# Kernel optimization log

Measured on AMD Instinct MI355X. Metric: run time of the kernel, lower is better.

The kernel has to match this reference:

```python
import jax, jax.numpy as jnp
import numpy as np

HEADS = 4
DIM_HEAD = 64
KS = 7
IN_CH = 256
OUT_CH = HEADS * DIM_HEAD


def setup_inputs() -> dict:
    key = jax.random.key(0)
    k1, k2, k3, k4, k5 = jax.random.split(key, 5)
    b, c, h, w = 2, IN_CH, 64, 64
    kvmap1 = jax.random.normal(k1, (b, c, h, w), dtype=jnp.float32)
    qmap = jax.random.normal(k2, (b, c, h, w), dtype=jnp.float32)
    kvmap2 = jax.random.normal(k3, (b, c, h, w), dtype=jnp.float32)
    # 1x1 conv weights [out_channels, in_channels], kaiming-ish scale
    Wq = jax.random.normal(k4, (OUT_CH, IN_CH), dtype=jnp.float32) * (1.0 / np.sqrt(IN_CH))
    Wkv = jax.random.normal(k5, (OUT_CH, IN_CH), dtype=jnp.float32) * (1.0 / np.sqrt(IN_CH))
    return {"kvmap1": kvmap1, "qmap": qmap, "kvmap2": kvmap2, "Wq": Wq, "Wkv": Wkv}


def _branch(kvmap, Wkv, q, h, w):
    # pad like F.pad([ks//2, (ks-1)//2, ks//2, (ks-1)//2])
    pl, pr = KS // 2, (KS - 1) // 2
    padded = jnp.pad(kvmap, ((0, 0), (0, 0), (pl, pr), (pl, pr)))
    kv = jnp.einsum('bchw,oc->bohw', padded, Wkv)  # 1x1 conv, k == v in the original
    b = kv.shape[0]
    # unfold: [b, C, ks*ks, h, w] with (k1, k2) row-major, matching torch unfold order
    patches = jnp.stack([kv[:, :, i:i + h, j:j + w]
                         for i in range(KS) for j in range(KS)], axis=2)
    k = patches.reshape(b, HEADS, DIM_HEAD, KS * KS, h * w)
    k = k.transpose(0, 1, 4, 3, 2)  # [b, n, hw, k^2, d]
    logits = jnp.einsum('bnxd,bnxyd->bnxy', q, k)
    wts = jax.nn.softmax(logits, axis=-1)
    return jnp.einsum('bnxy,bnxyd->bnxd', wts, k)  # v == k


def reference(kvmap1, qmap, kvmap2, Wq, Wkv):
    b, c, h, w = qmap.shape
    scale = DIM_HEAD ** (-0.5)
    q = jnp.einsum('bchw,oc->bohw', qmap, Wq) * scale
    q = q.reshape(b, HEADS, DIM_HEAD, h * w).transpose(0, 1, 3, 2)  # [b, n, hw, d]
    out1 = _branch(kvmap1, Wkv, q, h, w)
    out2 = _branch(kvmap2, Wkv, q, h, w)
    out = (out1 + out2) * 0.5  # [b, n, hw, d]
    return out.transpose(0, 1, 3, 2).reshape(b, HEADS * DIM_HEAD, h, w)
```

## Files before the change

kernel.cpp:

```cpp
#include <hip/hip_runtime.h>
#include <hip/hip_bf16.h>
#include <math.h>

#define HEADS 4
#define DH 64
#define CH 256
#define HW 4096
#define HH 64
#define WW 64
#define BB 2
#define KS 7

#define NPOS 224
#define ROWB 448
#define WROWB 256

typedef __attribute__((ext_vector_type(8))) short bf16x8;
typedef __attribute__((ext_vector_type(4))) float f32x4;
typedef __attribute__((ext_vector_type(4))) short short4_t;

__device__ __forceinline__ short f2bf(float x) {
  union { float f; unsigned u; } v; v.f = x;
  unsigned r = (v.u + 0x7fffu + ((v.u >> 16) & 1u)) >> 16;
  return (short)r;
}

__device__ __forceinline__ int swz(int row, int byte_off) {
  return byte_off ^ ((row & 7) << 4);
}

__global__ __launch_bounds__(256) void wcvt_kernel(
    const float* __restrict__ Wq, const float* __restrict__ Wkv,
    short* __restrict__ Wqb, short* __restrict__ Wkvb) {
  const int i = (blockIdx.x * 256 + threadIdx.x) * 4;
  const float* src = blockIdx.y ? Wkv : Wq;
  short* dst = blockIdx.y ? Wkvb : Wqb;
  const float sc = blockIdx.y ? 1.0f : 0.125f;
  float4 v = *(const float4*)(src + i);
  short4_t o;
  o.x = f2bf(v.x * sc); o.y = f2bf(v.y * sc);
  o.z = f2bf(v.z * sc); o.w = f2bf(v.w * sc);
  *(short4_t*)(dst + i) = o;
}

__global__ __launch_bounds__(256) void proj_mfma_kernel(
    const float* __restrict__ qmap, const float* __restrict__ kvmap1,
    const float* __restrict__ kvmap2, const short* __restrict__ Wqb,
    const short* __restrict__ Wkvb, short* __restrict__ Qt,
    short* __restrict__ KV1, short* __restrict__ KV2) {
  const float* in; const short* Wb; short* out;
  switch (blockIdx.z >> 2) {
    case 0:  in = qmap;   Wb = Wqb;  out = Qt;  break;
    case 1:  in = kvmap1; Wb = Wkvb; out = KV1; break;
    default: in = kvmap2; Wb = Wkvb; out = KV2; break;
  }
  __shared__ short wl[64 * 256];
  const int ng = blockIdx.z & 3;
  const int b = blockIdx.y, t = threadIdx.x;
  const int w = t >> 6, lane = t & 63, l15 = lane & 15, lg = lane >> 4;

  {
    const short* wsrc = Wb + (size_t)(ng * 64) * CH;
    #pragma unroll
    for (int i = 0; i < 8; ++i) {
      int idx = i * 256 + t;
      int o = idx >> 5, slot = idx & 31;
      bf16x8 v = *(const bf16x8*)(wsrc + o * CH + slot * 8);
      *(bf16x8*)((char*)wl + o * 512 + ((slot * 16) ^ ((o & 7) * 16))) = v;
    }
  }

  const int pix = blockIdx.x * 64 + w * 16 + l15;
  const float* inb = in + (size_t)b * CH * HW;
  bf16x8 a[8];
  #pragma unroll
  for (int k8 = 0; k8 < 8; ++k8) {
    #pragma unroll
    for (int j = 0; j < 8; ++j)
      a[k8][j] = f2bf(inb[(size_t)(k8 * 32 + lg * 8 + j) * HW + pix]);
  }
  __syncthreads();

  const int prow = blockIdx.x * 64 + w * 16 + lg * 4;
  short* ob = out + (size_t)b * HW * CH;
  #pragma unroll
  for (int nq = 0; nq < 4; ++nq) {
    const int nt = ng * 4 + nq;
    const int o = nq * 16 + l15;
    f32x4 acc = (f32x4)0.f;
    #pragma unroll
    for (int k8 = 0; k8 < 8; ++k8) {
      bf16x8 bfrag = *(const bf16x8*)((char*)wl + o * 512 +
                                      (((k8 * 4 + lg) * 16) ^ ((o & 7) * 16)));
      acc = __builtin_amdgcn_mfma_f32_16x16x32_bf16(a[k8], bfrag, acc, 0, 0, 0);
    }
    #pragma unroll
    for (int r = 0; r < 4; ++r)
      ob[(size_t)(prow + r) * CH + nt * 16 + l15] = f2bf(acc[r]);
  }
}

__global__ __launch_bounds__(256, 3) void attn_kernel(
    const short* __restrict__ Qt, const short* __restrict__ KV1,
    const short* __restrict__ KV2, float* __restrict__ out) {
  __shared__ char KVT[64 * ROWB];
  __shared__ char WT [64 * WROWB];

  const int t = threadIdx.x, lane = t & 63, w = t >> 6;
  const int l15 = lane & 15, lg = lane >> 4;
  const int tile = blockIdx.x;
  const int ty = tile >> 3, tx = tile & 7;
  const int bn = blockIdx.y, b = bn >> 2, n = bn & 3;

  bf16x8 qf0, qf1;
  {
    int p = w * 16 + l15;
    int gp = (ty * 8 + (p >> 3)) * 64 + tx * 8 + (p & 7);
    const short* qb = Qt + ((size_t)b * HW + gp) * CH + n * DH + lg * 8;
    qf0 = *(const bf16x8*)(qb);
    qf1 = *(const bf16x8*)(qb + 32);
  }

  f32x4 acc2[4];
  #pragma unroll
  for (int i = 0; i < 4; ++i) acc2[i] = (f32x4)0.f;

  const int p = w * 16 + l15, px = p & 7;
  const int hi8 = l15 >> 3;

  #pragma unroll
  for (int br = 0; br < 2; ++br) {
    const short* kv = (br ? KV2 : KV1) + (size_t)b * HW * CH + n * DH;
    if (br) __syncthreads();

    #pragma unroll
    for (int it = 0; it < 2; ++it) {
      int tid = it * 256 + t;
      if (tid < 448) {
        int dc = (tid * 586) >> 15;
        int posT = tid - dc * 56;
        int pos0 = posT * 4;
        int uy = pos0 >> 4, ux0 = pos0 & 15;
        int gy = ty * 8 + uy - 3;
        bool yok = (gy >= 0) && (gy < HH);
        bf16x8 v[4];
        #pragma unroll
        for (int r = 0; r < 4; ++r) {
          int ux = ux0 + r;
          int gx = tx * 8 + ux - 3;
          bool valid = yok && (ux < 14) && (gx >= 0) && (gx < WW);
          v[r] = (bf16x8)0;
          if (valid)
            v[r] = *(const bf16x8*)(kv + (size_t)(gy * WW + gx) * CH + dc * 8);
        }
        #pragma unroll
        for (int j = 0; j < 8; ++j) {
          int d = dc * 8 + j;
          short4_t pk;
          pk[0] = v[0][j]; pk[1] = v[1][j]; pk[2] = v[2][j]; pk[3] = v[3][j];
          *(short4_t*)(KVT + swz(d, d * ROWB + pos0 * 2)) = pk;
        }
      }
    }
    __syncthreads();

    f32x4 sa[8];
    {
      int ux = l15;
      int gx = tx * 8 + ux - 3;
      bool xok = (ux < 14) && (gx >= 0) && (gx < WW);
      #pragma unroll
      for (int i = 0; i < 8; ++i) {
        int gy = ty * 8 + (2 * w + i) - 3;
        bool valid = xok && (gy >= 0) && (gy < HH);
        bf16x8 a0 = (bf16x8)0, a1 = (bf16x8)0;
        if (valid) {
          const short* src = kv + (size_t)(gy * WW + gx) * CH + lg * 8;
          a0 = *(const bf16x8*)(src);
          a1 = *(const bf16x8*)(src + 32);
        }
        f32x4 s = (f32x4)0.f;
        s = __builtin_amdgcn_mfma_f32_16x16x32_bf16(a0, qf0, s, 0, 0, 0);
        s = __builtin_amdgcn_mfma_f32_16x16x32_bf16(a1, qf1, s, 0, 0, 0);
        sa[i] = s;
      }
    }

    float m = -1e30f;
    #pragma unroll
    for (int i = 0; i < 8; ++i) {
      int dy = i - hi8;
      bool yok = (dy >= 0) && (dy <= 6);
      #pragma unroll
      for (int r = 0; r < 4; ++r) {
        int dx = (lg * 4 + r) - px;
        bool in = yok && (dx >= 0) && (dx <= 6);
        float s = in ? sa[i][r] : -1e30f;
        sa[i][r] = s;
        m = fmaxf(m, s);
      }
    }
    m = fmaxf(m, __shfl_xor(m, 16, 64));
    m = fmaxf(m, __shfl_xor(m, 32, 64));
    float den = 0.f;
    #pragma unroll
    for (int i = 0; i < 8; ++i) {
      #pragma unroll
      for (int r = 0; r < 4; ++r) {
        float e = __expf(sa[i][r] - m);
        sa[i][r] = e;
        den += e;
      }
    }
    den += __shfl_xor(den, 16, 64);
    den += __shfl_xor(den, 32, 64);
    float inv = 1.f / den;

    #pragma unroll
    for (int i = 0; i < 8; ++i) {
      short4_t pk;
      #pragma unroll
      for (int r = 0; r < 4; ++r) pk[r] = f2bf(sa[i][r] * inv);
      *(short4_t*)(WT + swz(p, p * WROWB + (i * 16 + lg * 4) * 2)) = pk;
    }

    #pragma unroll 1
    for (int kp = 0; kp < 4; ++kp) {
      int lposb = (kp * 32 + lg * 8) * 2;
      int gposb = (32 * w + kp * 32 + lg * 8) * 2;
      bf16x8 af = *(const bf16x8*)(WT + swz(p, p * WROWB + lposb));
      #pragma unroll
      for (int ntp = 0; ntp < 4; ++ntp) {
        int brow = ntp * 16 + l15;
        bf16x8 bf = *(const bf16x8*)(KVT + swz(brow, brow * ROWB + gposb));
        acc2[ntp] = __builtin_amdgcn_mfma_f32_16x16x32_bf16(af, bf, acc2[ntp], 0, 0, 0);
      }
    }
  }

  int p0 = w * 16 + lg * 4;
  int gp = (ty * 8 + (p0 >> 3)) * 64 + tx * 8 + (p0 & 7);
  #pragma unroll
  for (int ntp = 0; ntp < 4; ++ntp) {
    int o = n * DH + ntp * 16 + l15;
    f32x4 v = acc2[ntp] * 0.5f;
    *(f32x4*)(out + ((size_t)b * CH + o) * HW + gp) = v;
  }
}

extern "C" void kernel_launch(void* const* d_in, const int* in_sizes, int n_in,
                              void* d_out, int out_size, void* d_ws, size_t ws_size,
                              hipStream_t stream) {
  const float* kvmap1 = (const float*)d_in[0];
  const float* qmap   = (const float*)d_in[1];
  const float* kvmap2 = (const float*)d_in[2];
  const float* Wq     = (const float*)d_in[3];
  const float* Wkv    = (const float*)d_in[4];
  float* out = (float*)d_out;

  short* Qt   = (short*)d_ws;
  short* KV1  = Qt  + (size_t)BB * HW * CH;
  short* KV2  = KV1 + (size_t)BB * HW * CH;
  short* Wqb  = KV2 + (size_t)BB * HW * CH;
  short* Wkvb = Wqb + (size_t)CH * CH;

  dim3 wgrid(64, 2);
  wcvt_kernel<<<wgrid, 256, 0, stream>>>(Wq, Wkv, Wqb, Wkvb);

  dim3 pgrid(HW / 64, BB, 12);
  proj_mfma_kernel<<<pgrid, 256, 0, stream>>>(qmap, kvmap1, kvmap2, Wqb, Wkvb,
                                              Qt, KV1, KV2);

  dim3 agrid(64, BB * HEADS);
  attn_kernel<<<agrid, 256, 0, stream>>>(Qt, KV1, KV2, out);
}
```

Baseline: 40.12 us.

## Fuse weight conversion into projection and keep softmax weights in registers

```diff
diff --git a/kernel.cpp b/kernel.cpp
--- a/kernel.cpp
+++ b/kernel.cpp
@@ -1,5 +1,4 @@
 #include <hip/hip_runtime.h>
-#include <hip/hip_bf16.h>
 #include <math.h>
 
 #define HEADS 4
@@ -9,11 +8,9 @@
 #define HH 64
 #define WW 64
 #define BB 2
-#define KS 7
 
 #define NPOS 224
 #define ROWB 448
-#define WROWB 256
 
 typedef __attribute__((ext_vector_type(8))) short bf16x8;
 typedef __attribute__((ext_vector_type(4))) float f32x4;
@@ -29,30 +26,16 @@
   return byte_off ^ ((row & 7) << 4);
 }
 
-__global__ __launch_bounds__(256) void wcvt_kernel(
-    const float* __restrict__ Wq, const float* __restrict__ Wkv,
-    short* __restrict__ Wqb, short* __restrict__ Wkvb) {
-  const int i = (blockIdx.x * 256 + threadIdx.x) * 4;
-  const float* src = blockIdx.y ? Wkv : Wq;
-  short* dst = blockIdx.y ? Wkvb : Wqb;
-  const float sc = blockIdx.y ? 1.0f : 0.125f;
-  float4 v = *(const float4*)(src + i);
-  short4_t o;
-  o.x = f2bf(v.x * sc); o.y = f2bf(v.y * sc);
-  o.z = f2bf(v.z * sc); o.w = f2bf(v.w * sc);
-  *(short4_t*)(dst + i) = o;
-}
-
 __global__ __launch_bounds__(256) void proj_mfma_kernel(
     const float* __restrict__ qmap, const float* __restrict__ kvmap1,
-    const float* __restrict__ kvmap2, const short* __restrict__ Wqb,
-    const short* __restrict__ Wkvb, short* __restrict__ Qt,
+    const float* __restrict__ kvmap2, const float* __restrict__ Wq,
+    const float* __restrict__ Wkv, short* __restrict__ Qt,
     short* __restrict__ KV1, short* __restrict__ KV2) {
-  const float* in; const short* Wb; short* out;
+  const float* in; const float* Wf; short* out; float wsc;
   switch (blockIdx.z >> 2) {
-    case 0:  in = qmap;   Wb = Wqb;  out = Qt;  break;
-    case 1:  in = kvmap1; Wb = Wkvb; out = KV1; break;
-    default: in = kvmap2; Wb = Wkvb; out = KV2; break;
+    case 0:  in = qmap;   Wf = Wq;  out = Qt;  wsc = 0.125f; break;
+    case 1:  in = kvmap1; Wf = Wkv; out = KV1; wsc = 1.0f;   break;
+    default: in = kvmap2; Wf = Wkv; out = KV2; wsc = 1.0f;   break;
   }
   __shared__ short wl[64 * 256];
   const int ng = blockIdx.z & 3;
@@ -60,13 +43,17 @@
   const int w = t >> 6, lane = t & 63, l15 = lane & 15, lg = lane >> 4;
 
   {
-    const short* wsrc = Wb + (size_t)(ng * 64) * CH;
-    #pragma unroll
-    for (int i = 0; i < 8; ++i) {
+    const float* wsrc = Wf + (size_t)(ng * 64) * CH;
+    #pragma unroll
+    for (int i = 0; i < 16; ++i) {
       int idx = i * 256 + t;
-      int o = idx >> 5, slot = idx & 31;
-      bf16x8 v = *(const bf16x8*)(wsrc + o * CH + slot * 8);
-      *(bf16x8*)((char*)wl + o * 512 + ((slot * 16) ^ ((o & 7) * 16))) = v;
+      int o = idx >> 6, q4 = idx & 63;
+      float4 v = *(const float4*)(wsrc + o * CH + q4 * 4);
+      short4_t pk;
+      pk[0] = f2bf(v.x * wsc); pk[1] = f2bf(v.y * wsc);
+      pk[2] = f2bf(v.z * wsc); pk[3] = f2bf(v.w * wsc);
+      int s = q4 >> 1, h = q4 & 1;
+      *(short4_t*)((char*)wl + o * 512 + ((s * 16) ^ ((o & 7) * 16)) + h * 8) = pk;
     }
   }
 
@@ -100,17 +87,16 @@
   }
 }
 
-__global__ __launch_bounds__(256, 3) void attn_kernel(
+__global__ __launch_bounds__(256, 4) void attn_kernel(
     const short* __restrict__ Qt, const short* __restrict__ KV1,
     const short* __restrict__ KV2, float* __restrict__ out) {
   __shared__ char KVT[64 * ROWB];
-  __shared__ char WT [64 * WROWB];
 
   const int t = threadIdx.x, lane = t & 63, w = t >> 6;
   const int l15 = lane & 15, lg = lane >> 4;
-  const int tile = blockIdx.x;
+  const int bn = blockIdx.x, b = bn >> 2, n = bn & 3;
+  const int tile = blockIdx.y;
   const int ty = tile >> 3, tx = tile & 7;
-  const int bn = blockIdx.y, b = bn >> 2, n = bn & 3;
 
   bf16x8 qf0, qf1;
   {
@@ -141,6 +127,7 @@
         int posT = tid - dc * 56;
         int pos0 = posT * 4;
         int uy = pos0 >> 4, ux0 = pos0 & 15;
+        int colp = 32 * (uy >> 1) + 8 * (ux0 >> 2) + 4 * (uy & 1);
         int gy = ty * 8 + uy - 3;
         bool yok = (gy >= 0) && (gy < HH);
         bf16x8 v[4];
@@ -158,7 +145,7 @@
           int d = dc * 8 + j;
           short4_t pk;
           pk[0] = v[0][j]; pk[1] = v[1][j]; pk[2] = v[2][j]; pk[3] = v[3][j];
-          *(short4_t*)(KVT + swz(d, d * ROWB + pos0 * 2)) = pk;
+          *(short4_t*)(KVT + swz(d, d * ROWB + colp * 2)) = pk;
         }
       }
     }
@@ -216,19 +203,18 @@
     den += __shfl_xor(den, 32, 64);
     float inv = 1.f / den;
 
+    short4_t pk4[8];
     #pragma unroll
     for (int i = 0; i < 8; ++i) {
-      short4_t pk;
-      #pragma unroll
-      for (int r = 0; r < 4; ++r) pk[r] = f2bf(sa[i][r] * inv);
-      *(short4_t*)(WT + swz(p, p * WROWB + (i * 16 + lg * 4) * 2)) = pk;
-    }
-
-    #pragma unroll 1
+      #pragma unroll
+      for (int r = 0; r < 4; ++r) pk4[i][r] = f2bf(sa[i][r] * inv);
+    }
+
+    #pragma unroll
     for (int kp = 0; kp < 4; ++kp) {
-      int lposb = (kp * 32 + lg * 8) * 2;
       int gposb = (32 * w + kp * 32 + lg * 8) * 2;
-      bf16x8 af = *(const bf16x8*)(WT + swz(p, p * WROWB + lposb));
+      short4_t lo = pk4[2 * kp], hi = pk4[2 * kp + 1];
+      bf16x8 af = {lo[0], lo[1], lo[2], lo[3], hi[0], hi[1], hi[2], hi[3]};
       #pragma unroll
       for (int ntp = 0; ntp < 4; ++ntp) {
         int brow = ntp * 16 + l15;
@@ -258,19 +244,14 @@
   const float* Wkv    = (const float*)d_in[4];
   float* out = (float*)d_out;
 
-  short* Qt   = (short*)d_ws;
-  short* KV1  = Qt  + (size_t)BB * HW * CH;
-  short* KV2  = KV1 + (size_t)BB * HW * CH;
-  short* Wqb  = KV2 + (size_t)BB * HW * CH;
-  short* Wkvb = Wqb + (size_t)CH * CH;
-
-  dim3 wgrid(64, 2);
-  wcvt_kernel<<<wgrid, 256, 0, stream>>>(Wq, Wkv, Wqb, Wkvb);
+  short* Qt  = (short*)d_ws;
+  short* KV1 = Qt  + (size_t)BB * HW * CH;
+  short* KV2 = KV1 + (size_t)BB * HW * CH;
 
   dim3 pgrid(HW / 64, BB, 12);
-  proj_mfma_kernel<<<pgrid, 256, 0, stream>>>(qmap, kvmap1, kvmap2, Wqb, Wkvb,
+  proj_mfma_kernel<<<pgrid, 256, 0, stream>>>(qmap, kvmap1, kvmap2, Wq, Wkv,
                                               Qt, KV1, KV2);
 
-  dim3 agrid(64, BB * HEADS);
+  dim3 agrid(BB * HEADS, 64);
   attn_kernel<<<agrid, 256, 0, stream>>>(Qt, KV1, KV2, out);
 }
```

Result: faster. 35.12 us (-12.5%).
